# Kernel optimization log

Hardware: AMD Instinct MI355X
Metric: run time of the kernel (lower is better)

## Reference

```python
import jax, jax.numpy as jnp
import numpy as np

B, L, D = 4, 4096, 768

def setup_inputs() -> dict:
    key = jax.random.key(0)
    ks = jax.random.split(key, 4)
    s = 1.0 / np.sqrt(D)
    return {
        "hidden_states": jax.random.normal(ks[0], (B, L, D), dtype=jnp.float32),
        "Wq": jax.random.normal(ks[1], (D, D), dtype=jnp.float32) * s,
        "bq": jnp.zeros((D,), dtype=jnp.float32),
        "Wk": jax.random.normal(ks[2], (D, D), dtype=jnp.float32) * s,
        "bk": jnp.zeros((D,), dtype=jnp.float32),
        "Wv": jax.random.normal(ks[3], (D, D), dtype=jnp.float32) * s,
        "bv": jnp.zeros((D,), dtype=jnp.float32),
    }

def reference(hidden_states, Wq, bq, Wk, bk, Wv, bv):
    # Linear projections (torch Linear: x @ W^T + b; here W stored as [in, out]-equivalent via transpose-free einsum)
    q = jnp.einsum('bld,de->ble', hidden_states, Wq) + bq
    k = jnp.einsum('bld,de->ble', hidden_states, Wk) + bk
    v = jnp.einsum('bld,de->ble', hidden_states, Wv) + bv
    # Single-head attention, NO 1/sqrt(d) scaling (faithful to source)
    weight = jnp.einsum('bqd,bkd->bqk', q, k)          # [B, L, L]
    weight = jax.nn.softmax(weight, axis=-1)
    score = jnp.einsum('bqk,bkd->bqd', weight, v)      # [B, L, D]
    return score
```

## Files before the change

kernel.cpp:

```cpp
#include <hip/hip_runtime.h>


typedef _Float16 f16;
typedef _Float16 f16x8 __attribute__((ext_vector_type(8)));
typedef _Float16 f16x4 __attribute__((ext_vector_type(4)));
typedef float f32x4 __attribute__((ext_vector_type(4)));

#define NB 4
#define NL 4096
#define ND 768
#define NM (NB * NL)

__device__ __forceinline__ void split_f16(float v, f16& h, f16& l) {
    h = (f16)v;
    l = (f16)(v - (float)h);
}

__global__ __launch_bounds__(256) void k_convert_x(
    const float* __restrict__ x, f16* __restrict__ xh, f16* __restrict__ xl) {
    int i = blockIdx.x * 256 + threadIdx.x;
    float4 v = ((const float4*)x)[i];
    float vv[4] = {v.x, v.y, v.z, v.w};
    f16x4 hv, lv;
    for (int j = 0; j < 4; ++j) {
        f16 h, l; split_f16(vv[j], h, l);
        hv[j] = h; lv[j] = l;
    }
    ((f16x4*)xh)[i] = hv;
    ((f16x4*)xl)[i] = lv;
}

__global__ __launch_bounds__(256) void k_convert_w(
    const float* __restrict__ Wq, const float* __restrict__ Wk,
    const float* __restrict__ Wv, f16* __restrict__ wth, f16* __restrict__ wtl) {
    __shared__ float tile[32][33];
    const float* W = blockIdx.z == 0 ? Wq : (blockIdx.z == 1 ? Wk : Wv);
    f16* th = wth + blockIdx.z * ND * ND;
    f16* tl = wtl + blockIdx.z * ND * ND;
    const int k0 = blockIdx.x * 32, n0 = blockIdx.y * 32;
    const int tx = threadIdx.x & 31, ty = threadIdx.x >> 5;
    for (int r = 0; r < 4; ++r)
        tile[r * 8 + ty][tx] = W[(k0 + r * 8 + ty) * ND + n0 + tx];
    __syncthreads();
    for (int r = 0; r < 4; ++r) {
        float v = tile[tx][r * 8 + ty];
        int n = n0 + r * 8 + ty, k = k0 + tx;
        f16 h, l; split_f16(v, h, l);
        th[n * ND + k] = h;
        tl[n * ND + k] = l;
    }
}

__global__ __launch_bounds__(256, 2) void k_proj(
    const f16* __restrict__ xh, const f16* __restrict__ xl,
    const f16* __restrict__ wth, const f16* __restrict__ wtl,
    const float* __restrict__ bq, const float* __restrict__ bk,
    const float* __restrict__ bv,
    f16* __restrict__ qh, f16* __restrict__ kh, f16* __restrict__ vt) {
    const int z = blockIdx.z;
    const f16* wh = wth + z * ND * ND;
    const f16* wl = wtl + z * ND * ND;
    const float* bias = z == 0 ? bq : (z == 1 ? bk : bv);
    const int m0 = blockIdx.x * 128, n0 = blockIdx.y * 128;

    __shared__ f16 Ah[128 * 40], Al[128 * 40], Bh[128 * 40], Bl[128 * 40];

    const int t = threadIdx.x;
    const int lane = t & 63, quad = lane >> 4, l16 = lane & 15;
    const int wave = t >> 6, wm = wave >> 1, wn = wave & 1;

    f32x4 acc[4][4] = {};

    for (int kt = 0; kt < 24; ++kt) {
        const int k0 = kt * 32;
        __syncthreads();
        for (int i = 0; i < 2; ++i) {
            int c = i * 256 + t;
            int row = c >> 2, kc = (c & 3) * 8;
            *(uint4*)&Ah[row * 40 + kc] = *(const uint4*)&xh[(m0 + row) * ND + k0 + kc];
            *(uint4*)&Al[row * 40 + kc] = *(const uint4*)&xl[(m0 + row) * ND + k0 + kc];
            *(uint4*)&Bh[row * 40 + kc] = *(const uint4*)&wh[(n0 + row) * ND + k0 + kc];
            *(uint4*)&Bl[row * 40 + kc] = *(const uint4*)&wl[(n0 + row) * ND + k0 + kc];
        }
        __syncthreads();
        f16x8 ah[4], al[4], bh[4], bl[4];
#pragma unroll
        for (int f = 0; f < 4; ++f) {
            int m = wm * 64 + f * 16 + l16;
            ah[f] = *(const f16x8*)&Ah[m * 40 + quad * 8];
            al[f] = *(const f16x8*)&Al[m * 40 + quad * 8];
            int n = wn * 64 + f * 16 + l16;
            bh[f] = *(const f16x8*)&Bh[n * 40 + quad * 8];
            bl[f] = *(const f16x8*)&Bl[n * 40 + quad * 8];
        }
#pragma unroll
        for (int fm = 0; fm < 4; ++fm)
#pragma unroll
            for (int fn = 0; fn < 4; ++fn) {
                f32x4 c = acc[fm][fn];
                c = __builtin_amdgcn_mfma_f32_16x16x32_f16(al[fm], bh[fn], c, 0, 0, 0);
                c = __builtin_amdgcn_mfma_f32_16x16x32_f16(ah[fm], bl[fn], c, 0, 0, 0);
                c = __builtin_amdgcn_mfma_f32_16x16x32_f16(ah[fm], bh[fn], c, 0, 0, 0);
                acc[fm][fn] = c;
            }
    }
#pragma unroll
    for (int fm = 0; fm < 4; ++fm)
#pragma unroll
        for (int fn = 0; fn < 4; ++fn) {
            int col = n0 + wn * 64 + fn * 16 + l16;
            float bv_ = bias[col];
#pragma unroll
            for (int r = 0; r < 4; ++r) {
                int row = m0 + wm * 64 + fm * 16 + quad * 4 + r;
                float v = acc[fm][fn][r] + bv_;
                f16 h = (f16)v;
                if (z == 0) { qh[row * ND + col] = h; }
                else if (z == 1) { kh[row * ND + col] = h; }
                else {
                    int b = row >> 12, pos = row & 4095;
                    vt[(b * ND + col) * NL + pos] = h;
                }
            }
        }
}

__global__ __launch_bounds__(512, 2) void k_attn(
    const f16* __restrict__ qh, const f16* __restrict__ kh,
    const f16* __restrict__ vt, float* __restrict__ out) {
    const int qt = blockIdx.x, b = blockIdx.y;
    const int q0 = qt * 64;
    const int t = threadIdx.x, w = t >> 6, lane = t & 63;
    const int quad = lane >> 4, l16 = lane & 15;
    const int dw = w * 96;
    const int kvw = w * 16;

    __shared__ f16 Qbuf[64 * 776];
    __shared__ f16 Pbuf[64 * 136];
    __shared__ float mwT[64][12];
    __shared__ float psT[64][12];

    for (int c = t; c < 6144; c += 512) {
        int row = c / 96, col8 = (c % 96) * 8;
        *(uint4*)&Qbuf[row * 776 + col8] =
            *(const uint4*)&qh[(b * NL + q0 + row) * ND + col8];
    }
    float mreg[4][4], lreg[4][4];
#pragma unroll
    for (int fm = 0; fm < 4; ++fm)
#pragma unroll
        for (int r = 0; r < 4; ++r) { mreg[fm][r] = -1e30f; lreg[fm][r] = 0.f; }
    f32x4 oacc[4][6] = {};
    __syncthreads();

    for (int kt = 0; kt < 32; ++kt) {
        const int p0 = kt * 128;

        f16x8 vb[2][6];
#pragma unroll
        for (int fn = 0; fn < 6; ++fn)
            vb[0][fn] = *(const f16x8*)&vt[(b * ND + dw + fn * 16 + l16) * NL +
                                           p0 + quad * 8];

        f32x4 sacc[4] = {};
#pragma unroll
        for (int ks = 0; ks < 24; ++ks) {
            const int d = ks * 32 + quad * 8;
            f16x8 bH = *(const f16x8*)&kh[(b * NL + p0 + kvw + l16) * ND + d];
#pragma unroll
            for (int fm = 0; fm < 4; ++fm) {
                f16x8 aH = *(const f16x8*)&Qbuf[(fm * 16 + l16) * 776 + d];
                sacc[fm] = __builtin_amdgcn_mfma_f32_16x16x32_f16(aH, bH, sacc[fm], 0, 0, 0);
            }
        }

#pragma unroll
        for (int fm = 0; fm < 4; ++fm)
#pragma unroll
            for (int r = 0; r < 4; ++r) {
                float v = sacc[fm][r];
#pragma unroll
                for (int off = 1; off < 16; off <<= 1) v = fmaxf(v, __shfl_xor(v, off, 64));
                if (l16 == 0) mwT[fm * 16 + quad * 4 + r][w] = v;
            }
        __syncthreads();

        float alpha[4][4];
#pragma unroll
        for (int fm = 0; fm < 4; ++fm)
#pragma unroll
            for (int r = 0; r < 4; ++r) {
                const int row = fm * 16 + quad * 4 + r;
                f32x4 a4 = *(const f32x4*)&mwT[row][0];
                f32x4 b4 = *(const f32x4*)&mwT[row][4];
                float tmax = fmaxf(fmaxf(fmaxf(a4[0], a4[1]), fmaxf(a4[2], a4[3])),
                                   fmaxf(fmaxf(b4[0], b4[1]), fmaxf(b4[2], b4[3])));
                float m_new = fmaxf(mreg[fm][r], tmax);
                alpha[fm][r] = __expf(mreg[fm][r] - m_new);
                mreg[fm][r] = m_new;
                float p = __expf(sacc[fm][r] - m_new);
                Pbuf[row * 136 + kvw + l16] = (f16)p;
#pragma unroll
                for (int off = 1; off < 16; off <<= 1) p += __shfl_xor(p, off, 64);
                if (l16 == 0) psT[row][w] = p;
            }
        __syncthreads();

#pragma unroll
        for (int fm = 0; fm < 4; ++fm)
#pragma unroll
            for (int r = 0; r < 4; ++r) {
                const int row = fm * 16 + quad * 4 + r;
                f32x4 a4 = *(const f32x4*)&psT[row][0];
                f32x4 b4 = *(const f32x4*)&psT[row][4];
                lreg[fm][r] = alpha[fm][r] * lreg[fm][r] +
                              ((a4[0] + a4[1]) + (a4[2] + a4[3])) +
                              ((b4[0] + b4[1]) + (b4[2] + b4[3]));
#pragma unroll
                for (int fn = 0; fn < 6; ++fn) oacc[fm][fn][r] *= alpha[fm][r];
            }

#pragma unroll
        for (int ks = 0; ks < 4; ++ks) {
            if (ks < 3) {
#pragma unroll
                for (int fn = 0; fn < 6; ++fn)
                    vb[(ks + 1) & 1][fn] =
                        *(const f16x8*)&vt[(b * ND + dw + fn * 16 + l16) * NL +
                                           p0 + (ks + 1) * 32 + quad * 8];
            }
            f16x8 pa[4];
#pragma unroll
            for (int fm = 0; fm < 4; ++fm)
                pa[fm] = *(const f16x8*)&Pbuf[(fm * 16 + l16) * 136 + ks * 32 + quad * 8];
#pragma unroll
            for (int fn = 0; fn < 6; ++fn)
#pragma unroll
                for (int fm = 0; fm < 4; ++fm)
                    oacc[fm][fn] = __builtin_amdgcn_mfma_f32_16x16x32_f16(
                        pa[fm], vb[ks & 1][fn], oacc[fm][fn], 0, 0, 0);
        }
    }

#pragma unroll
    for (int fm = 0; fm < 4; ++fm)
#pragma unroll
        for (int fn = 0; fn < 6; ++fn) {
            int col = dw + fn * 16 + l16;
#pragma unroll
            for (int r = 0; r < 4; ++r) {
                int row = b * NL + q0 + fm * 16 + quad * 4 + r;
                out[row * ND + col] = oacc[fm][fn][r] / lreg[fm][r];
            }
        }
}

extern "C" void kernel_launch(void* const* d_in, const int* in_sizes, int n_in,
                              void* d_out, int out_size, void* d_ws, size_t ws_size,
                              hipStream_t stream) {
    const float* hs = (const float*)d_in[0];
    const float* Wq = (const float*)d_in[1];
    const float* bq = (const float*)d_in[2];
    const float* Wk = (const float*)d_in[3];
    const float* bk = (const float*)d_in[4];
    const float* Wv = (const float*)d_in[5];
    const float* bv = (const float*)d_in[6];
    float* out = (float*)d_out;

    char* ws = (char*)d_ws;
    size_t off = 0;
    auto alloc = [&](size_t bytes) {
        void* p = ws + off;
        off += (bytes + 255) & ~(size_t)255;
        return p;
    };
    const size_t MD = (size_t)NM * ND;
    f16* Xh = (f16*)alloc(MD * 2);
    f16* Xl = (f16*)alloc(MD * 2);
    f16* Wth = (f16*)alloc((size_t)3 * ND * ND * 2);
    f16* Wtl = (f16*)alloc((size_t)3 * ND * ND * 2);
    f16* Qh = (f16*)alloc(MD * 2);
    f16* Kh = (f16*)alloc(MD * 2);
    f16* Vt = (f16*)alloc(MD * 2);
    (void)ws_size; (void)in_sizes; (void)n_in; (void)out_size;

    k_convert_x<<<dim3(MD / 1024), 256, 0, stream>>>(hs, Xh, Xl);
    k_convert_w<<<dim3(24, 24, 3), 256, 0, stream>>>(Wq, Wk, Wv, Wth, Wtl);
    k_proj<<<dim3(NM / 128, ND / 128, 3), 256, 0, stream>>>(
        Xh, Xl, Wth, Wtl, bq, bk, bv, Qh, Kh, Vt);
    k_attn<<<dim3(NL / 64, NB), 512, 0, stream>>>(Qh, Kh, Vt, out);
}
```

Before: 831.3 us.

## Double KV tile to 256 keys and software-pipeline K fragment loads

Each wave now computes scores for 32 keys instead of 16, so the KV tile grows to 256 and the loop runs 16 times instead of 32. This halves the number of barrier and softmax-reduction rounds per key and reuses each Q fragment read from LDS across two MFMAs. K fragments are prefetched two steps ahead through a register double buffer that carries into the next tile. The cost is more registers per thread (extra accumulators and prefetch buffers) and a larger P buffer in LDS, which may hurt occupancy under the 2-blocks-per-CU launch bound.

Measured after the change: 903.2 us. +8.6%, slower.

```diff
diff --git a/kernel.cpp b/kernel.cpp
--- a/kernel.cpp
+++ b/kernel.cpp
@@ -133,12 +133,23 @@
     const int t = threadIdx.x, w = t >> 6, lane = t & 63;
     const int quad = lane >> 4, l16 = lane & 15;
     const int dw = w * 96;
-    const int kvw = w * 16;
+    const int kvw = w * 32;
 
     __shared__ f16 Qbuf[64 * 776];
-    __shared__ f16 Pbuf[64 * 136];
+    __shared__ f16 Pbuf[64 * 264];
     __shared__ float mwT[64][12];
     __shared__ float psT[64][12];
+
+    const f16* kbase = &kh[(b * NL + kvw + l16) * ND];
+    const f16* kbase2 = &kh[(b * NL + kvw + 16 + l16) * ND];
+
+    f16x8 bK[2][2];
+#pragma unroll
+    for (int ks = 0; ks < 2; ++ks) {
+        const int d = ks * 32 + quad * 8;
+        bK[ks][0] = *(const f16x8*)&kbase[d];
+        bK[ks][1] = *(const f16x8*)&kbase2[d];
+    }
 
     for (int c = t; c < 6144; c += 512) {
         int row = c / 96, col8 = (c % 96) * 8;
@@ -153,8 +164,8 @@
     f32x4 oacc[4][6] = {};
     __syncthreads();
 
-    for (int kt = 0; kt < 32; ++kt) {
-        const int p0 = kt * 128;
+    for (int kt = 0; kt < 16; ++kt) {
+        const int p0 = kt * 256;
 
         f16x8 vb[2][6];
 #pragma unroll
@@ -162,15 +173,24 @@
             vb[0][fn] = *(const f16x8*)&vt[(b * ND + dw + fn * 16 + l16) * NL +
                                            p0 + quad * 8];
 
-        f32x4 sacc[4] = {};
+        f32x4 sacc[4][2] = {};
 #pragma unroll
         for (int ks = 0; ks < 24; ++ks) {
+            const f16x8 b0 = bK[ks & 1][0], b1 = bK[ks & 1][1];
+            {
+                const int ks2 = ks + 2;
+                const int row_off = (ks2 >= 24) ? 256 : 0;
+                const int d2 = ((ks2 >= 24) ? ks2 - 24 : ks2) * 32 + quad * 8;
+                const long ofs = (long)(p0 + row_off) * ND + d2;
+                bK[ks & 1][0] = *(const f16x8*)&kbase[ofs];
+                bK[ks & 1][1] = *(const f16x8*)&kbase2[ofs];
+            }
             const int d = ks * 32 + quad * 8;
-            f16x8 bH = *(const f16x8*)&kh[(b * NL + p0 + kvw + l16) * ND + d];
 #pragma unroll
             for (int fm = 0; fm < 4; ++fm) {
                 f16x8 aH = *(const f16x8*)&Qbuf[(fm * 16 + l16) * 776 + d];
-                sacc[fm] = __builtin_amdgcn_mfma_f32_16x16x32_f16(aH, bH, sacc[fm], 0, 0, 0);
+                sacc[fm][0] = __builtin_amdgcn_mfma_f32_16x16x32_f16(aH, b0, sacc[fm][0], 0, 0, 0);
+                sacc[fm][1] = __builtin_amdgcn_mfma_f32_16x16x32_f16(aH, b1, sacc[fm][1], 0, 0, 0);
             }
         }
 
@@ -178,7 +198,7 @@
         for (int fm = 0; fm < 4; ++fm)
 #pragma unroll
             for (int r = 0; r < 4; ++r) {
-                float v = sacc[fm][r];
+                float v = fmaxf(sacc[fm][0][r], sacc[fm][1][r]);
 #pragma unroll
                 for (int off = 1; off < 16; off <<= 1) v = fmaxf(v, __shfl_xor(v, off, 64));
                 if (l16 == 0) mwT[fm * 16 + quad * 4 + r][w] = v;
@@ -198,11 +218,14 @@
                 float m_new = fmaxf(mreg[fm][r], tmax);
                 alpha[fm][r] = __expf(mreg[fm][r] - m_new);
                 mreg[fm][r] = m_new;
-                float p = __expf(sacc[fm][r] - m_new);
-                Pbuf[row * 136 + kvw + l16] = (f16)p;
-#pragma unroll
-                for (int off = 1; off < 16; off <<= 1) p += __shfl_xor(p, off, 64);
-                if (l16 == 0) psT[row][w] = p;
+                float p0v = __expf(sacc[fm][0][r] - m_new);
+                float p1v = __expf(sacc[fm][1][r] - m_new);
+                Pbuf[row * 264 + kvw + l16] = (f16)p0v;
+                Pbuf[row * 264 + kvw + 16 + l16] = (f16)p1v;
+                float ps = p0v + p1v;
+#pragma unroll
+                for (int off = 1; off < 16; off <<= 1) ps += __shfl_xor(ps, off, 64);
+                if (l16 == 0) psT[row][w] = ps;
             }
         __syncthreads();
 
@@ -221,8 +244,8 @@
             }
 
 #pragma unroll
-        for (int ks = 0; ks < 4; ++ks) {
-            if (ks < 3) {
+        for (int ks = 0; ks < 8; ++ks) {
+            if (ks < 7) {
 #pragma unroll
                 for (int fn = 0; fn < 6; ++fn)
                     vb[(ks + 1) & 1][fn] =
@@ -232,7 +255,7 @@
             f16x8 pa[4];
 #pragma unroll
             for (int fm = 0; fm < 4; ++fm)
-                pa[fm] = *(const f16x8*)&Pbuf[(fm * 16 + l16) * 136 + ks * 32 + quad * 8];
+                pa[fm] = *(const f16x8*)&Pbuf[(fm * 16 + l16) * 264 + ks * 32 + quad * 8];
 #pragma unroll
             for (int fn = 0; fn < 6; ++fn)
 #pragma unroll
```

## Use 16-wave attention blocks with 256-key tiles and halved per-wave output width

Applied to the files above, without the earlier changes.

The attention kernel now runs 1024 threads (16 waves) per block instead of 512. Each wave owns 16 keys of a 256-key tile and 48 output columns, so there are half as many KV iterations and barriers per key. The V prefetch double buffer is dropped in favour of loading V directly each step. Register pressure per wave falls, but shared memory and cross-wave reductions grow, and the launch bounds no longer request two blocks per CU.

Measured after the change: 905.3 us. 8.9% more time.

```diff
diff --git a/kernel.cpp b/kernel.cpp
--- a/kernel.cpp
+++ b/kernel.cpp
@@ -125,22 +125,24 @@
         }
 }
 
-__global__ __launch_bounds__(512, 2) void k_attn(
+__global__ __launch_bounds__(1024) void k_attn(
     const f16* __restrict__ qh, const f16* __restrict__ kh,
     const f16* __restrict__ vt, float* __restrict__ out) {
     const int qt = blockIdx.x, b = blockIdx.y;
     const int q0 = qt * 64;
     const int t = threadIdx.x, w = t >> 6, lane = t & 63;
     const int quad = lane >> 4, l16 = lane & 15;
-    const int dw = w * 96;
+    const int dw = w * 48;
     const int kvw = w * 16;
 
     __shared__ f16 Qbuf[64 * 776];
-    __shared__ f16 Pbuf[64 * 136];
-    __shared__ float mwT[64][12];
-    __shared__ float psT[64][12];
-
-    for (int c = t; c < 6144; c += 512) {
+    __shared__ f16 Pbuf[64 * 264];
+    __shared__ float mwT[64][20];
+    __shared__ float psT[64][20];
+
+    const f16* kbase = &kh[((size_t)b * NL + kvw + l16) * ND];
+
+    for (int c = t; c < 6144; c += 1024) {
         int row = c / 96, col8 = (c % 96) * 8;
         *(uint4*)&Qbuf[row * 776 + col8] =
             *(const uint4*)&qh[(b * NL + q0 + row) * ND + col8];
@@ -150,27 +152,22 @@
     for (int fm = 0; fm < 4; ++fm)
 #pragma unroll
         for (int r = 0; r < 4; ++r) { mreg[fm][r] = -1e30f; lreg[fm][r] = 0.f; }
-    f32x4 oacc[4][6] = {};
+    f32x4 oacc[4][3] = {};
     __syncthreads();
 
-    for (int kt = 0; kt < 32; ++kt) {
-        const int p0 = kt * 128;
-
-        f16x8 vb[2][6];
-#pragma unroll
-        for (int fn = 0; fn < 6; ++fn)
-            vb[0][fn] = *(const f16x8*)&vt[(b * ND + dw + fn * 16 + l16) * NL +
-                                           p0 + quad * 8];
+    for (int kt = 0; kt < 16; ++kt) {
+        const int p0 = kt * 256;
+        const f16* kb1 = kbase + (size_t)p0 * ND;
 
         f32x4 sacc[4] = {};
 #pragma unroll
         for (int ks = 0; ks < 24; ++ks) {
             const int d = ks * 32 + quad * 8;
-            f16x8 bH = *(const f16x8*)&kh[(b * NL + p0 + kvw + l16) * ND + d];
+            const f16x8 b0 = *(const f16x8*)&kb1[d];
 #pragma unroll
             for (int fm = 0; fm < 4; ++fm) {
                 f16x8 aH = *(const f16x8*)&Qbuf[(fm * 16 + l16) * 776 + d];
-                sacc[fm] = __builtin_amdgcn_mfma_f32_16x16x32_f16(aH, bH, sacc[fm], 0, 0, 0);
+                sacc[fm] = __builtin_amdgcn_mfma_f32_16x16x32_f16(aH, b0, sacc[fm], 0, 0, 0);
             }
         }
 
@@ -193,13 +190,18 @@
                 const int row = fm * 16 + quad * 4 + r;
                 f32x4 a4 = *(const f32x4*)&mwT[row][0];
                 f32x4 b4 = *(const f32x4*)&mwT[row][4];
-                float tmax = fmaxf(fmaxf(fmaxf(a4[0], a4[1]), fmaxf(a4[2], a4[3])),
-                                   fmaxf(fmaxf(b4[0], b4[1]), fmaxf(b4[2], b4[3])));
+                f32x4 c4 = *(const f32x4*)&mwT[row][8];
+                f32x4 d4 = *(const f32x4*)&mwT[row][12];
+                float t1 = fmaxf(fmaxf(a4[0], a4[1]), fmaxf(a4[2], a4[3]));
+                float t2 = fmaxf(fmaxf(b4[0], b4[1]), fmaxf(b4[2], b4[3]));
+                float t3 = fmaxf(fmaxf(c4[0], c4[1]), fmaxf(c4[2], c4[3]));
+                float t4 = fmaxf(fmaxf(d4[0], d4[1]), fmaxf(d4[2], d4[3]));
+                float tmax = fmaxf(fmaxf(t1, t2), fmaxf(t3, t4));
                 float m_new = fmaxf(mreg[fm][r], tmax);
                 alpha[fm][r] = __expf(mreg[fm][r] - m_new);
                 mreg[fm][r] = m_new;
                 float p = __expf(sacc[fm][r] - m_new);
-                Pbuf[row * 136 + kvw + l16] = (f16)p;
+                Pbuf[row * 264 + kvw + l16] = (f16)p;
 #pragma unroll
                 for (int off = 1; off < 16; off <<= 1) p += __shfl_xor(p, off, 64);
                 if (l16 == 0) psT[row][w] = p;
@@ -213,39 +215,41 @@
                 const int row = fm * 16 + quad * 4 + r;
                 f32x4 a4 = *(const f32x4*)&psT[row][0];
                 f32x4 b4 = *(const f32x4*)&psT[row][4];
-                lreg[fm][r] = alpha[fm][r] * lreg[fm][r] +
-                              ((a4[0] + a4[1]) + (a4[2] + a4[3])) +
-                              ((b4[0] + b4[1]) + (b4[2] + b4[3]));
-#pragma unroll
-                for (int fn = 0; fn < 6; ++fn) oacc[fm][fn][r] *= alpha[fm][r];
-            }
-
-#pragma unroll
-        for (int ks = 0; ks < 4; ++ks) {
-            if (ks < 3) {
-#pragma unroll
-                for (int fn = 0; fn < 6; ++fn)
-                    vb[(ks + 1) & 1][fn] =
-                        *(const f16x8*)&vt[(b * ND + dw + fn * 16 + l16) * NL +
-                                           p0 + (ks + 1) * 32 + quad * 8];
-            }
+                f32x4 c4 = *(const f32x4*)&psT[row][8];
+                f32x4 d4 = *(const f32x4*)&psT[row][12];
+                float s1 = (a4[0] + a4[1]) + (a4[2] + a4[3]);
+                float s2 = (b4[0] + b4[1]) + (b4[2] + b4[3]);
+                float s3 = (c4[0] + c4[1]) + (c4[2] + c4[3]);
+                float s4 = (d4[0] + d4[1]) + (d4[2] + d4[3]);
+                lreg[fm][r] = alpha[fm][r] * lreg[fm][r] + ((s1 + s2) + (s3 + s4));
+#pragma unroll
+                for (int fn = 0; fn < 3; ++fn) oacc[fm][fn][r] *= alpha[fm][r];
+            }
+
+#pragma unroll
+        for (int ks = 0; ks < 8; ++ks) {
+            f16x8 vb[3];
+#pragma unroll
+            for (int fn = 0; fn < 3; ++fn)
+                vb[fn] = *(const f16x8*)&vt[(b * ND + dw + fn * 16 + l16) * NL +
+                                            p0 + ks * 32 + quad * 8];
             f16x8 pa[4];
 #pragma unroll
             for (int fm = 0; fm < 4; ++fm)
-                pa[fm] = *(const f16x8*)&Pbuf[(fm * 16 + l16) * 136 + ks * 32 + quad * 8];
-#pragma unroll
-            for (int fn = 0; fn < 6; ++fn)
+                pa[fm] = *(const f16x8*)&Pbuf[(fm * 16 + l16) * 264 + ks * 32 + quad * 8];
+#pragma unroll
+            for (int fn = 0; fn < 3; ++fn)
 #pragma unroll
                 for (int fm = 0; fm < 4; ++fm)
                     oacc[fm][fn] = __builtin_amdgcn_mfma_f32_16x16x32_f16(
-                        pa[fm], vb[ks & 1][fn], oacc[fm][fn], 0, 0, 0);
+                        pa[fm], vb[fn], oacc[fm][fn], 0, 0, 0);
         }
     }
 
 #pragma unroll
     for (int fm = 0; fm < 4; ++fm)
 #pragma unroll
-        for (int fn = 0; fn < 6; ++fn) {
+        for (int fn = 0; fn < 3; ++fn) {
             int col = dw + fn * 16 + l16;
 #pragma unroll
             for (int r = 0; r < 4; ++r) {
@@ -288,5 +292,5 @@
     k_convert_w<<<dim3(24, 24, 3), 256, 0, stream>>>(Wq, Wk, Wv, Wth, Wtl);
     k_proj<<<dim3(NM / 128, ND / 128, 3), 256, 0, stream>>>(
         Xh, Xl, Wth, Wtl, bq, bk, bv, Qh, Kh, Vt);
-    k_attn<<<dim3(NL / 64, NB), 512, 0, stream>>>(Qh, Kh, Vt, out);
-}
+    k_attn<<<dim3(NL / 64, NB), 1024, 0, stream>>>(Qh, Kh, Vt, out);
+}
```
